# Optimization experiments

Measured on AMD Instinct MI355X. Metric: run time of the kernel, lower is better.

The kernel has to match this reference:

```python
import jax, jax.numpy as jnp
import numpy as np
from jax.scipy.special import logsumexp

S, D, K, R, P = 500, 768, 16, 256, 64  # seq_len, bert_dim, out_dim, n_pairs, max wordpieces/entity


def setup_inputs() -> dict:
    key = jax.random.key(0)
    k1, k2, k3, k4, k5, k6 = jax.random.split(key, 6)
    word_embeddings = jax.random.normal(k1, (S, D), jnp.float32)
    # kaiming_normal_ fan_in = D*K (last two dims collapsed); gain sqrt(2) for relu
    W = jax.random.normal(k2, (D, K, D), jnp.float32) * np.float32((2.0 / (K * D)) ** 0.5)
    idx1 = jax.random.randint(k3, (R, P), 0, S)
    idx2 = jax.random.randint(k4, (R, P), 0, S)
    # ragged mention lengths -> padding masks (at least 1 valid wordpiece)
    len1 = jax.random.randint(k5, (R,), 1, P + 1)
    len2 = jax.random.randint(k6, (R,), 1, P + 1)
    pos = jnp.arange(P)
    mask1 = (pos[None, :] < len1[:, None]).astype(jnp.float32)
    mask2 = (pos[None, :] < len2[:, None]).astype(jnp.float32)
    return {"word_embeddings": word_embeddings, "W": W, "idx1": idx1, "idx2": idx2,
            "mask1": mask1, "mask2": mask2}


def reference(word_embeddings, W, idx1, idx2, mask1, mask2):
    # gather ragged mention wordpieces (padded to P per entity)
    e1 = word_embeddings[idx1]  # [R, P, D]
    e2 = word_embeddings[idx2]  # [R, P, D]
    # biaffine: z[r,k,p,q] = e1[r,p,:] @ W[:,k,:] @ e2[r,q,:]
    zh = jnp.einsum('rpd,dke->rpke', e1, W)      # [R, P, K, D]
    z = jnp.einsum('rpke,rqe->rkpq', zh, e2)     # [R, K, P, P]
    # logsumexp pooling over all valid (p, q) mention-token pairs
    b = mask1[:, None, :, None] * mask2[:, None, None, :]  # [R, 1, P, P]
    scores = logsumexp(z, axis=(2, 3), b=b)      # [R, K]
    return scores
```

## Files before the change

### kernel.cpp

```cpp
#include <hip/hip_runtime.h>
#include <math.h>

#define S_ 500
#define D_ 768
#define K_ 16
#define R_ 256
#define P_ 64
#define NT 12

typedef unsigned short ushort_t;
typedef __attribute__((ext_vector_type(8))) short short8;
typedef __attribute__((ext_vector_type(4))) float floatx4;

__device__ inline ushort_t f2bf(float x) {
  unsigned int u = __float_as_uint(x);
  u += 0x7fffu + ((u >> 16) & 1u);
  return (ushort_t)(u >> 16);
}

#define GLD_LDS16(g, l)                                                        \
  __builtin_amdgcn_global_load_lds(                                            \
      (const __attribute__((address_space(1))) void*)(g),                      \
      (__attribute__((address_space(3))) void*)(l), 16, 0, 0)

#define ASM_BARRIER asm volatile("s_barrier" ::: "memory")
#define WAIT_VM8 asm volatile("s_waitcnt vmcnt(8)" ::: "memory")
#define WAIT_VM6 asm volatile("s_waitcnt vmcnt(6)" ::: "memory")
#define WAIT_VM0 asm volatile("s_waitcnt vmcnt(0)" ::: "memory")

__global__ __launch_bounds__(256) void prep(const float* __restrict__ WE,
                                            const float* __restrict__ W,
                                            ushort_t* __restrict__ WEb,
                                            ushort_t* __restrict__ Wt) {
  const int t = threadIdx.x;
  if (blockIdx.x < 384) {
    int gid = blockIdx.x * 256 + t;
    int row = gid / 192;
    ushort4 o = {0, 0, 0, 0};
    if (row < S_) {
      float4 v = *(const float4*)(WE + (size_t)gid * 4);
      o.x = f2bf(v.x); o.y = f2bf(v.y); o.z = f2bf(v.z); o.w = f2bf(v.w);
    }
    *(ushort4*)(WEb + (size_t)gid * 4) = o;
    return;
  }
  __shared__ float tile[64][68];
  const int tb = blockIdx.x - 384;
  const int n0 = (tb % 192) * 64, d0 = (tb / 192) * 64;
  {
    const int r = t >> 2, cbase = (t & 3) * 16;
#pragma unroll
    for (int i = 0; i < 4; i++) {
      float4 v = *(const float4*)(W + (size_t)(d0 + r) * 12288 + n0 + cbase + i * 4);
      *(float4*)&tile[r][cbase + i * 4] = v;
    }
  }
  __syncthreads();
  {
    const int bc = t & 15;
    const int br4 = (t >> 4) * 4;
    float4 tv[4];
#pragma unroll
    for (int ii = 0; ii < 4; ii++)
      tv[ii] = *(const float4*)&tile[bc * 4 + ii][br4];
#pragma unroll
    for (int j = 0; j < 4; j++) {
      ushort4 o;
      o.x = f2bf(((const float*)&tv[0])[j]);
      o.y = f2bf(((const float*)&tv[1])[j]);
      o.z = f2bf(((const float*)&tv[2])[j]);
      o.w = f2bf(((const float*)&tv[3])[j]);
      *(ushort4*)(Wt + (size_t)(n0 + br4 + j) * 768 + d0 + bc * 4) = o;
    }
  }
}

__global__ __launch_bounds__(256, 2) void mm0_bt(const ushort_t* __restrict__ A,
                                                 const ushort_t* __restrict__ Bm,
                                                 ushort_t* __restrict__ C) {
  __shared__ ushort_t As[2][2][128 * 32];
  __shared__ ushort_t Bs[2][2][128 * 32];
  const int tid = threadIdx.x;
  const int wave = tid >> 6, lane = tid & 63;
  const int m0 = blockIdx.y * 128, n0 = blockIdx.x * 128;
  const int wm = (wave & 1) * 64, wn = (wave >> 1) * 64;
  const int col = lane & 15, quad = lane >> 4;

  floatx4 acc[4][4];
#pragma unroll
  for (int i = 0; i < 4; i++)
#pragma unroll
    for (int j = 0; j < 4; j++)
#pragma unroll
      for (int e = 0; e < 4; e++) acc[i][j][e] = 0.f;

  const int srow = wave * 32 + (lane >> 2);
  const int scol = (lane & 3) * 8;
  const ushort_t* ga0 = A + (size_t)(m0 + srow) * D_ + scol;
  const ushort_t* gb0 = Bm + (size_t)(n0 + srow) * D_ + scol;
  const int ldsbase = (wave * 32) * 32;

#define ISSUE_TILE0(t_, buf_)                                                  \
  do {                                                                         \
    const ushort_t* ga = ga0 + (t_)*64;                                        \
    const ushort_t* gb = gb0 + (t_)*64;                                        \
    GLD_LDS16(ga, &As[buf_][0][ldsbase]);                                      \
    GLD_LDS16(ga + 16 * D_, &As[buf_][0][ldsbase + 16 * 32]);                  \
    GLD_LDS16(ga + 32, &As[buf_][1][ldsbase]);                                 \
    GLD_LDS16(ga + 32 + 16 * D_, &As[buf_][1][ldsbase + 16 * 32]);             \
    GLD_LDS16(gb, &Bs[buf_][0][ldsbase]);                                      \
    GLD_LDS16(gb + 16 * D_, &Bs[buf_][0][ldsbase + 16 * 32]);                  \
    GLD_LDS16(gb + 32, &Bs[buf_][1][ldsbase]);                                 \
    GLD_LDS16(gb + 32 + 16 * D_, &Bs[buf_][1][ldsbase + 16 * 32]);             \
  } while (0)

  ISSUE_TILE0(0, 0);
  for (int t = 0; t < NT; ++t) {
    const int cur = t & 1;
    if (t + 1 < NT) {
      ISSUE_TILE0(t + 1, cur ^ 1);
      WAIT_VM8;
    } else {
      WAIT_VM0;
    }
    ASM_BARRIER;
#pragma unroll
    for (int s = 0; s < 2; ++s) {
      short8 a[4], b[4];
#pragma unroll
      for (int i = 0; i < 4; i++)
        a[i] = *(const short8*)&As[cur][s][(wm + i * 16 + col) * 32 + quad * 8];
#pragma unroll
      for (int j = 0; j < 4; j++)
        b[j] = *(const short8*)&Bs[cur][s][(wn + j * 16 + col) * 32 + quad * 8];
#pragma unroll
      for (int i = 0; i < 4; i++)
#pragma unroll
        for (int j = 0; j < 4; j++)
          acc[i][j] = __builtin_amdgcn_mfma_f32_16x16x32_bf16(b[j], a[i], acc[i][j], 0, 0, 0);
    }
    ASM_BARRIER;
  }
#undef ISSUE_TILE0

#pragma unroll
  for (int i = 0; i < 4; i++) {
    int m = m0 + wm + i * 16 + col;
#pragma unroll
    for (int j = 0; j < 4; j++) {
      int n = n0 + wn + j * 16 + quad * 4;
      ushort4 o;
      o.x = f2bf(acc[i][j][0]); o.y = f2bf(acc[i][j][1]);
      o.z = f2bf(acc[i][j][2]); o.w = f2bf(acc[i][j][3]);
      *(ushort4*)(C + (size_t)m * 12288 + n) = o;
    }
  }
}

__global__ __launch_bounds__(256, 2) void mm1_bt(const ushort_t* __restrict__ A,
                                                 const ushort_t* __restrict__ Bm,
                                                 ushort_t* __restrict__ G) {
  __shared__ ushort_t As[2][2][128 * 32];
  __shared__ ushort_t Bs[2][2][64 * 32];
  const int tid = threadIdx.x;
  const int wave = tid >> 6, lane = tid & 63;
  const int m0 = blockIdx.y * 128, n0 = blockIdx.x * 64;
  const int wm = (wave & 1) * 64, wn = (wave >> 1) * 32;
  const int col = lane & 15, quad = lane >> 4;

  floatx4 acc[4][2];
#pragma unroll
  for (int i = 0; i < 4; i++)
#pragma unroll
    for (int j = 0; j < 2; j++)
#pragma unroll
      for (int e = 0; e < 4; e++) acc[i][j][e] = 0.f;

  const int lrow = lane >> 2, scol = (lane & 3) * 8;
  const ushort_t* ga0 = A + (size_t)(m0 + wave * 32 + lrow) * D_ + scol;
  const ushort_t* gb0 = Bm + (size_t)(n0 + wave * 16 + lrow) * D_ + scol;
  const int aoff = (wave * 32) * 32;
  const int boff = (wave * 16) * 32;

#define ISSUE_TILE1(t_, buf_)                                                  \
  do {                                                                         \
    _Pragma("unroll") for (int s_ = 0; s_ < 2; s_++) {                         \
      const ushort_t* ga = ga0 + (t_)*64 + s_ * 32;                            \
      const ushort_t* gb = gb0 + (t_)*64 + s_ * 32;                            \
      GLD_LDS16(ga, &As[buf_][s_][aoff]);                                      \
      GLD_LDS16(ga + 16 * D_, &As[buf_][s_][aoff + 16 * 32]);                  \
      GLD_LDS16(gb, &Bs[buf_][s_][boff]);                                      \
    }                                                                          \
  } while (0)

  ISSUE_TILE1(0, 0);
  for (int t = 0; t < NT; ++t) {
    const int cur = t & 1;
    if (t + 1 < NT) {
      ISSUE_TILE1(t + 1, cur ^ 1);
      WAIT_VM6;
    } else {
      WAIT_VM0;
    }
    ASM_BARRIER;
#pragma unroll
    for (int s = 0; s < 2; ++s) {
      short8 a[4], b[2];
#pragma unroll
      for (int i = 0; i < 4; i++)
        a[i] = *(const short8*)&As[cur][s][(wm + i * 16 + col) * 32 + quad * 8];
#pragma unroll
      for (int j = 0; j < 2; j++)
        b[j] = *(const short8*)&Bs[cur][s][(wn + j * 16 + col) * 32 + quad * 8];
#pragma unroll
      for (int i = 0; i < 4; i++)
#pragma unroll
        for (int j = 0; j < 2; j++)
          acc[i][j] = __builtin_amdgcn_mfma_f32_16x16x32_bf16(a[i], b[j], acc[i][j], 0, 0, 0);
    }
    ASM_BARRIER;
  }
#undef ISSUE_TILE1

#pragma unroll
  for (int i = 0; i < 4; i++) {
    int s1 = (m0 + wm + i * 16) >> 4;
#pragma unroll
    for (int j = 0; j < 2; j++) {
      int s2 = n0 + wn + j * 16 + col;
      if (s1 < S_ && s2 < S_) {
        ushort4 o;
        o.x = f2bf(acc[i][j][0]); o.y = f2bf(acc[i][j][1]);
        o.z = f2bf(acc[i][j][2]); o.w = f2bf(acc[i][j][3]);
        *(ushort4*)(G + (((size_t)s1 * S_ + s2) << 4) + quad * 4) = o;
      }
    }
  }
}

__global__ __launch_bounds__(256) void lse_kernel(const ushort_t* __restrict__ G,
                                                  const int* __restrict__ idx1,
                                                  const int* __restrict__ idx2,
                                                  const float* __restrict__ mask1,
                                                  const float* __restrict__ mask2,
                                                  float* __restrict__ out) {
  const int r = blockIdx.x;
  const int tid = threadIdx.x;
  __shared__ int b1[P_], b2[P_];
  __shared__ int s_len1, s_len2;
  __shared__ float wmx[4][K_], wsum[4][K_];

  if (tid < 64) {
    float mv = mask1[r * P_ + tid];
    unsigned long long bal = __ballot(mv > 0.5f);
    if (tid == 0) s_len1 = (int)__popcll(bal);
    b1[tid] = idx1[r * P_ + tid] * (S_ * K_);
  } else if (tid < 128) {
    int q = tid - 64;
    float mv = mask2[r * P_ + q];
    unsigned long long bal = __ballot(mv > 0.5f);
    if (q == 0) s_len2 = (int)__popcll(bal);
    b2[q] = idx2[r * P_ + q] * K_;
  }
  __syncthreads();
  const int len2 = s_len2;
  const int total = s_len1 * len2;

  float m[K_], s[K_];
#pragma unroll
  for (int k = 0; k < K_; k++) { m[k] = -3.0e38f; s[k] = 0.f; }

  for (int i = tid; i < total; i += 256) {
    int p = i / len2;
    int q = i - p * len2;
    const uint4* g4 = (const uint4*)(G + b1[p] + b2[q]);
    uint4 w0 = g4[0], w1 = g4[1];
    unsigned int uu[8] = {w0.x, w0.y, w0.z, w0.w, w1.x, w1.y, w1.z, w1.w};
    float z[K_];
#pragma unroll
    for (int h = 0; h < 8; h++) {
      z[2 * h + 0] = __uint_as_float(uu[h] << 16);
      z[2 * h + 1] = __uint_as_float(uu[h] & 0xffff0000u);
    }
#pragma unroll
    for (int k = 0; k < K_; k++) {
      float zk = z[k];
      float M2 = fmaxf(m[k], zk);
      s[k] = s[k] * __expf(m[k] - M2) + __expf(zk - M2);
      m[k] = M2;
    }
  }

#pragma unroll
  for (int off = 1; off < 64; off <<= 1) {
#pragma unroll
    for (int k = 0; k < K_; k++) {
      float mo = __shfl_xor(m[k], off, 64);
      float so = __shfl_xor(s[k], off, 64);
      float M2 = fmaxf(m[k], mo);
      s[k] = s[k] * __expf(m[k] - M2) + so * __expf(mo - M2);
      m[k] = M2;
    }
  }
  const int wave = tid >> 6, lane = tid & 63;
  if (lane == 0) {
#pragma unroll
    for (int k = 0; k < K_; k++) { wmx[wave][k] = m[k]; wsum[wave][k] = s[k]; }
  }
  __syncthreads();
  if (tid < K_) {
    float M = -3.0e38f, Ssum = 0.f;
#pragma unroll
    for (int w = 0; w < 4; w++) {
      float mo = wmx[w][tid], so = wsum[w][tid];
      float M2 = fmaxf(M, mo);
      Ssum = Ssum * __expf(M - M2) + so * __expf(mo - M2);
      M = M2;
    }
    out[r * K_ + tid] = M + __logf(Ssum);
  }
}

extern "C" void kernel_launch(void* const* d_in, const int* in_sizes, int n_in,
                              void* d_out, int out_size, void* d_ws, size_t ws_size,
                              hipStream_t stream) {
  const float* WE    = (const float*)d_in[0];
  const float* W     = (const float*)d_in[1];
  const int*   idx1  = (const int*)d_in[2];
  const int*   idx2  = (const int*)d_in[3];
  const float* mask1 = (const float*)d_in[4];
  const float* mask2 = (const float*)d_in[5];
  float* out = (float*)d_out;

  ushort_t* WEb   = (ushort_t*)d_ws;
  ushort_t* Wt    = WEb + (size_t)512 * 768;
  ushort_t* projb = Wt + (size_t)12288 * 768;
  ushort_t* G     = projb + (size_t)8192 * 768;

  prep<<<384 + 2304, 256, 0, stream>>>(WE, W, WEb, Wt);
  mm0_bt<<<dim3(96, 4), 256, 0, stream>>>(WEb, Wt, projb);
  mm1_bt<<<dim3(8, 64), 256, 0, stream>>>(projb, WEb, G);
  lse_kernel<<<R_, 256, 0, stream>>>(G, idx1, idx2, mask1, mask2, out);
}
```

Measured before the change: 143.9 us.

## Swizzle mm1 block order, widen LSE blocks, use single-exp online logsumexp

Three separate changes. mm1_bt blocks are remapped through a swizzled linear index so that consecutive blocks share row and column tiles, aiming for better L2 reuse. lse_kernel moves from 256 to 512 threads per block, with 8 partial results per block, to put more loads in flight across only 256 blocks. The online logsumexp update now computes one exp of minus the absolute difference instead of two exps, which halves transcendental work but adds a select on every step.

After: 134.0 us. -6.9%, faster.

```diff
diff --git a/kernel.cpp b/kernel.cpp
--- a/kernel.cpp
+++ b/kernel.cpp
@@ -164,7 +164,10 @@
   __shared__ ushort_t Bs[2][2][64 * 32];
   const int tid = threadIdx.x;
   const int wave = tid >> 6, lane = tid & 63;
-  const int m0 = blockIdx.y * 128, n0 = blockIdx.x * 64;
+  const int lin = blockIdx.x + (blockIdx.y << 3);
+  const int yb = ((lin & 7) << 3) | (lin >> 6);
+  const int xb = (lin >> 3) & 7;
+  const int m0 = yb * 128, n0 = xb * 64;
   const int wm = (wave & 1) * 64, wn = (wave >> 1) * 32;
   const int col = lane & 15, quad = lane >> 4;
 
@@ -238,7 +241,7 @@
   }
 }
 
-__global__ __launch_bounds__(256) void lse_kernel(const ushort_t* __restrict__ G,
+__global__ __launch_bounds__(512) void lse_kernel(const ushort_t* __restrict__ G,
                                                   const int* __restrict__ idx1,
                                                   const int* __restrict__ idx2,
                                                   const float* __restrict__ mask1,
@@ -248,7 +251,7 @@
   const int tid = threadIdx.x;
   __shared__ int b1[P_], b2[P_];
   __shared__ int s_len1, s_len2;
-  __shared__ float wmx[4][K_], wsum[4][K_];
+  __shared__ float wmx[8][K_], wsum[8][K_];
 
   if (tid < 64) {
     float mv = mask1[r * P_ + tid];
@@ -270,7 +273,7 @@
 #pragma unroll
   for (int k = 0; k < K_; k++) { m[k] = -3.0e38f; s[k] = 0.f; }
 
-  for (int i = tid; i < total; i += 256) {
+  for (int i = tid; i < total; i += 512) {
     int p = i / len2;
     int q = i - p * len2;
     const uint4* g4 = (const uint4*)(G + b1[p] + b2[q]);
@@ -284,10 +287,11 @@
     }
 #pragma unroll
     for (int k = 0; k < K_; k++) {
-      float zk = z[k];
-      float M2 = fmaxf(m[k], zk);
-      s[k] = s[k] * __expf(m[k] - M2) + __expf(zk - M2);
-      m[k] = M2;
+      float d = z[k] - m[k];
+      float e = __expf(-fabsf(d));
+      bool up = d > 0.f;
+      s[k] = up ? __fmaf_rn(s[k], e, 1.f) : (s[k] + e);
+      m[k] = up ? z[k] : m[k];
     }
   }
 
@@ -297,9 +301,11 @@
     for (int k = 0; k < K_; k++) {
       float mo = __shfl_xor(m[k], off, 64);
       float so = __shfl_xor(s[k], off, 64);
-      float M2 = fmaxf(m[k], mo);
-      s[k] = s[k] * __expf(m[k] - M2) + so * __expf(mo - M2);
-      m[k] = M2;
+      float d = mo - m[k];
+      float e = __expf(-fabsf(d));
+      bool up = d > 0.f;
+      s[k] = up ? __fmaf_rn(s[k], e, so) : __fmaf_rn(so, e, s[k]);
+      m[k] = up ? mo : m[k];
     }
   }
   const int wave = tid >> 6, lane = tid & 63;
@@ -311,11 +317,13 @@
   if (tid < K_) {
     float M = -3.0e38f, Ssum = 0.f;
 #pragma unroll
-    for (int w = 0; w < 4; w++) {
+    for (int w = 0; w < 8; w++) {
       float mo = wmx[w][tid], so = wsum[w][tid];
-      float M2 = fmaxf(M, mo);
-      Ssum = Ssum * __expf(M - M2) + so * __expf(mo - M2);
-      M = M2;
+      float d = mo - M;
+      float e = __expf(-fabsf(d));
+      bool up = d > 0.f;
+      Ssum = up ? __fmaf_rn(Ssum, e, so) : __fmaf_rn(so, e, Ssum);
+      M = up ? mo : M;
     }
     out[r * K_ + tid] = M + __logf(Ssum);
   }
@@ -340,5 +348,5 @@
   prep<<<384 + 2304, 256, 0, stream>>>(WE, W, WEb, Wt);
   mm0_bt<<<dim3(96, 4), 256, 0, stream>>>(WEb, Wt, projb);
   mm1_bt<<<dim3(8, 64), 256, 0, stream>>>(projb, WEb, G);
-  lse_kernel<<<R_, 256, 0, stream>>>(G, idx1, idx2, mask1, mask2, out);
-}
+  lse_kernel<<<R_, 512, 0, stream>>>(G, idx1, idx2, mask1, mask2, out);
+}
```
